# Performance work log

Hardware: AMD Instinct MI355X
Metric: run time of the kernel (lower is better)

The kernel has to match this reference:

```python
import jax, jax.numpy as jnp
import numpy as np

K = 10          # neighbors per span
KTOK = 3        # heads used per span
D = 2.0         # token adjacency threshold
GAMMA = 1.0
MAX_WIDTH = 16
CAP = 128       # cap_spans_per_token
B, L, KTOK_TOTAL = 8, 128, 4


def _enumerate_spans(L, max_width):
    ar = np.arange(L)
    l_g, r_g = np.meshgrid(ar, ar, indexing='ij')
    mask = (r_g >= l_g) & (r_g - l_g + 1 <= max_width)
    l_idx = l_g[mask]
    r_idx = r_g[mask]
    S = l_idx.size
    span2id = np.full((L, L), -1, dtype=np.int64)
    span2id[l_idx, r_idx] = np.arange(S)
    return span2id, l_idx, r_idx, S


def _geom_matrix(L, max_width, span2id, l_idx, r_idx):
    # 8-neighborhood (l+/-1, r+/-1) adjacency over span ids, boolean (S,S)
    S = l_idx.size
    off = np.array([[-1, -1], [-1, 0], [-1, 1], [0, -1], [0, 1], [1, -1], [1, 0], [1, 1]])
    nl = l_idx[:, None] + off[None, :, 0]
    nr = r_idx[:, None] + off[None, :, 1]
    valid = (nl >= 0) & (nr >= 0) & (nl <= nr) & (nr < L) & (nr - nl + 1 <= max_width)
    s2 = span2id[np.clip(nl, 0, L - 1), np.clip(nr, 0, L - 1)]
    rows = np.broadcast_to(np.arange(S)[:, None], s2.shape)
    m = valid & (s2 >= 0)
    Geom = np.zeros((S, S), dtype=bool)
    Geom[rows[m], s2[m]] = True
    np.fill_diagonal(Geom, False)
    return Geom


SPAN2ID, L_IDX, R_IDX, S = _enumerate_spans(L, MAX_WIDTH)
GEOM = jnp.asarray(_geom_matrix(L, MAX_WIDTH, SPAN2ID, L_IDX, R_IDX))


def setup_inputs() -> dict:
    key = jax.random.key(0)
    k1, k2, k3 = jax.random.split(key, 3)
    head_indices = jax.random.randint(k1, (B, L, L, KTOK_TOTAL), 0, L)
    head_weights = jax.random.uniform(k2, (B, L, L, KTOK_TOTAL), dtype=jnp.float32)
    dist = jax.random.uniform(k3, (B, L, L), dtype=jnp.float32) * 8.0
    return {"head_indices": head_indices, "head_weights": head_weights, "dist": dist}


def reference(head_indices, head_weights, dist):
    l_idx = jnp.asarray(L_IDX)
    r_idx = jnp.asarray(R_IDX)
    # gather per-span head indices/weights: (B, S, Ktok)
    idx_all = head_indices[:, l_idx, r_idx, :KTOK]
    w_all = head_weights[:, l_idx, r_idx, :KTOK]
    valid1 = idx_all >= 0
    idx_safe = jnp.clip(idx_all, 0, None)
    w_all = w_all * valid1.astype(w_all.dtype)

    # scatter-add token->span dense matrices: (B, S, L)
    b_ix = jnp.arange(B)[:, None, None]
    s_ix = jnp.arange(S)[None, :, None]
    P_w = jnp.zeros((B, S, L), w_all.dtype).at[b_ix, s_ix, idx_safe].add(w_all)
    P_bin = jnp.zeros((B, S, L), jnp.float32).at[b_ix, s_ix, idx_safe].add(valid1.astype(jnp.float32))

    # token adjacency with self loops
    A = jnp.maximum((dist <= D).astype(jnp.float32), jnp.eye(L, dtype=jnp.float32))
    U_mask = jnp.einsum('bsl,blm->bsm', P_bin, A) > 0.0  # (B, S, L) spans hitting token m

    # top-1 head token -> span one-hot, with per-token span cap
    top1 = jnp.clip(idx_all[:, :, 0], 0, L - 1)
    top1_valid = (idx_all[:, :, 0] >= 0).astype(jnp.float32)
    E = jax.nn.one_hot(top1, L, dtype=jnp.float32) * top1_valid[..., None]  # (B, S, L)
    E = jnp.swapaxes(E, 1, 2)  # (B, L, S)
    E = E * (jnp.cumsum(E, axis=2) <= float(CAP)).astype(jnp.float32)

    # candidate matrix M: (B, S, S)
    M = jnp.einsum('bsl,blt->bst', U_mask.astype(jnp.float32), E) > 0.0
    diag = jnp.arange(S)
    M = M.at[:, diag, diag].set(False)
    M = M | GEOM[None]

    # gate scores Gate = P_w @ exp(-gamma*dist) @ P_w^T
    G = jnp.exp(-GAMMA * dist)
    A_pw = jnp.einsum('bsl,blm->bsm', P_w, G)
    Gate = jnp.einsum('bsm,btm->bst', A_pw, P_w)

    Gate_masked = jnp.where(M, Gate, -jnp.inf)
    topk_vals, topk_idx = jax.lax.top_k(Gate_masked, K)  # (B, S, K)
    N_mask = jnp.isfinite(topk_vals)
    N_idx = topk_idx.astype(jnp.int32)

    # self-loop fill for invalid slots
    rows = jnp.broadcast_to(jnp.arange(S, dtype=N_idx.dtype)[None, :, None], (B, S, K))
    N_idx = jnp.where(N_mask, N_idx, rows)
    N_mask = jnp.ones_like(N_mask)
    return N_idx, N_mask
```

## Files before the change

### kernel.cpp

```cpp
#include <hip/hip_runtime.h>
#include <stdint.h>

#define NB 8
#define LL 128
#define NS 1928
#define NK 10
#define WPB 4

__device__ __forceinline__ int span_id(int l, int r) {
    int off = (l <= 112) ? (l << 4) : (NS - (((128 - l) * (129 - l)) >> 1));
    return off + (r - l);
}

__device__ __forceinline__ float npexp_f32(float x) {
    const float magic = 12582912.0f;
    const float log2e = 1.442695040888963f;
    const float c1 = -6.93145752e-1f;
    const float c2 = -1.42860677e-6f;
    float t = __fmul_rn(x, log2e);
    float q = __fsub_rn(__fadd_rn(t, magic), magic);
    float r = __fmaf_rn(q, c1, x);
    r = __fmaf_rn(q, c2, r);
    float num = __fmaf_rn(r, 5.082762527590693718096e-04f, 6.757896990527504603057e-03f);
    num = __fmaf_rn(num, r, 5.114512081637298353406e-02f);
    num = __fmaf_rn(num, r, 2.473615434895520810817e-01f);
    num = __fmaf_rn(num, r, 7.257664613233124478488e-01f);
    num = __fmaf_rn(num, r, 9.999999999980870924916e-01f);
    float den = __fmaf_rn(r, 2.159509375685829852307e-02f, -2.742335390411667452936e-01f);
    den = __fmaf_rn(den, r, 1.0f);
    float p = __fdiv_rn(num, den);
    int qi = (int)q;
    return __fmul_rn(p, __int_as_float((127 + qi) << 23));
}

__device__ __forceinline__ float keyval(unsigned long long k) {
    return __uint_as_float((unsigned)(k >> 32));
}

__device__ __forceinline__ void wfence() {
    __builtin_amdgcn_wave_barrier();
    __threadfence_block();
    __builtin_amdgcn_wave_barrier();
}

__device__ int wave_partition_fast(unsigned long long* a, int* posL, int* posR,
                                   int pl, int pr, int lane) {
    int pm = pl + ((pr - pl) >> 1);
    unsigned long long vl = a[pl], vm = a[pm], vr = a[pr], tt;
    if (keyval(vm) < keyval(vl)) { tt = vm; vm = vl; vl = tt; }
    if (keyval(vr) < keyval(vm)) { tt = vr; vr = vm; vm = tt; }
    if (keyval(vm) < keyval(vl)) { tt = vm; vm = vl; vl = tt; }
    float vp = keyval(vm);
    unsigned long long vq = a[pr - 1];
    if (lane == 0) { a[pl] = vl; a[pr] = vr; a[pm] = vq; a[pr - 1] = vm; }
    wfence();

    unsigned long long lmask = (1ull << lane) - 1ull;
    int baseL = 0, baseR = 0;
    for (int p0 = pl; p0 <= pr; p0 += 64) {
        int pos = p0 + lane;
        bool inr = (pos <= pr);
        float v = inr ? keyval(a[pos]) : 0.0f;
        bool ge = inr && (pos > pl) && (pos < pr) && (v >= vp);
        bool le = inr && (pos <= pr - 2) && (v <= vp);
        unsigned long long bge = __ballot(ge);
        unsigned long long ble = __ballot(le);
        if (ge) posL[baseL + __popcll(bge & lmask)] = pos;
        if (le) posR[baseR + __popcll(ble & lmask)] = pos;
        baseL += __popcll(bge);
        baseR += __popcll(ble);
    }
    wfence();
    int totGE = baseL, totLE = baseR;
    int maxk = (totGE < totLE) ? totGE : totLE;
    int K = 0;
    for (int base = 0;; base += 64) {
        int k = base + lane;
        bool active = (k < maxk);
        int Lk = active ? posL[k] : 0x7fffffff;
        int Rk = active ? posR[totLE - 1 - k] : -1;
        bool sw = active && (Lk < Rk);
        unsigned long long bm = __ballot(sw);
        int nsw = (~bm == 0ull) ? 64 : (__ffsll((long long)~bm) - 1);
        if (sw && (lane < nsw)) {
            unsigned long long tl = a[Lk], tr = a[Rk];
            a[Lk] = tr; a[Rk] = tl;
        }
        K += nsw;
        if (nsw < 64) break;
    }
    wfence();
    int pi = posL[K];
    if (K > 0) { int rp = posR[totLE - K]; if (rp < pi) pi = rp; }
    if (lane == 0) { tt = a[pi]; a[pi] = a[pr - 1]; a[pr - 1] = tt; }
    wfence();
    return pi;
}

__device__ __forceinline__ void lane_sift(unsigned long long* h, int start, int hm) {
    unsigned long long tmp = h[start];
    int i = start, j = start + start;
    while (j <= hm) {
        if (j < hm && keyval(h[j]) < keyval(h[j + 1])) ++j;
        if (keyval(tmp) < keyval(h[j])) { h[i] = h[j]; i = j; j += j; }
        else break;
    }
    h[i] = tmp;
}

__device__ void wave_heap_top(unsigned long long* a, int lo, int hi, int needlo, int lane) {
    unsigned long long* h = a + lo - 1;
    int hm = hi - lo + 1;
    int half = hm >> 1;
    int maxlvl = 0; { int v = half; while (v >>= 1) ++maxlvl; }
    for (int lvl = maxlvl; lvl >= 0; --lvl) {
        int n0 = 1 << lvl;
        int n1 = (n0 << 1) - 1; if (n1 > half) n1 = half;
        for (int nb = n0; nb <= n1; nb += 64) {
            int node = nb + lane;
            if (node <= n1) lane_sift(h, node, hm);
        }
        wfence();
    }
    int E = hi - needlo + 1;
    if (E > hm - 1) E = hm - 1;
    if (lane == 0) {
        int m = hm;
        for (int e = 0; e < E; ++e) {
            unsigned long long tmp = h[m]; h[m] = h[1]; --m;
            int i = 1, j = 2;
            while (j <= m) {
                if (j < m && keyval(h[j]) < keyval(h[j + 1])) ++j;
                if (keyval(tmp) < keyval(h[j])) { h[i] = h[j]; i = j; j += j; }
                else break;
            }
            h[i] = tmp;
        }
    }
    wfence();
}

__device__ void wave_insertion(unsigned long long* a, int lo, int hi, int lane) {
    int len = hi - lo + 1;
    unsigned long long v = (lane < len) ? a[lo + lane] : 0ull;
    float fv = keyval(v);
    int rank = 0;
    for (int j = 0; j < len; ++j) {
        unsigned long long vj = __shfl(v, j, 64);
        float fj = keyval(vj);
        if ((fj < fv) || (fj == fv && j < lane)) ++rank;
    }
    wfence();
    if (lane < len) a[lo + rank] = v;
    wfence();
}

__device__ void wave_np_sort_top(unsigned long long* a, int n, int lane, int* stk,
                                 int* posL, int* posR) {
    int depth = 0; { int v = n; while (v >>= 1) ++depth; }
    depth *= 2;
    const int TOPLO = n - NK;
    int sp = 0;
    int lo = 0, hi = n - 1;
    for (;;) {
        while (hi - lo > 15) {
            if (depth-- < 0) {
                if (hi >= TOPLO) wave_heap_top(a, lo, hi, (lo > TOPLO ? lo : TOPLO), lane);
                goto pop;
            }
            {
                int pi = wave_partition_fast(a, posL, posR, lo, hi, lane);
                if (pi - lo < hi - pi) {
                    if (lane == 0) { stk[sp * 2] = pi + 1; stk[sp * 2 + 1] = hi; }
                    ++sp; hi = pi - 1;
                } else {
                    if (lane == 0) { stk[sp * 2] = lo; stk[sp * 2 + 1] = pi - 1; }
                    ++sp; lo = pi + 1;
                }
                wfence();
            }
        }
        if (hi > lo && hi >= TOPLO) wave_insertion(a, lo, hi, lane);
pop:
        if (sp == 0) break;
        --sp;
        lo = stk[sp * 2]; hi = stk[sp * 2 + 1];
    }
}

__global__ void top1_kernel(const int* __restrict__ hi,
                            unsigned char* __restrict__ top1,
                            unsigned char* __restrict__ flags) {
    int tid = blockIdx.x * blockDim.x + threadIdx.x;
    if (tid >= NB * NS) return;
    int b = tid / NS, t = tid - b * NS;
    int l, r;
    if (t < 1808) { l = t >> 4; r = l + (t & 15); }
    else {
        l = 113;
        while (l < 127 && span_id(l + 1, l + 1) <= t) ++l;
        r = l + (t - span_id(l, l));
    }
    int i0 = hi[((b * LL + l) * LL + r) * 4];
    top1[b * NS + t] = (unsigned char)(i0 & 127);
    flags[b * NS + t] = 0;
}

__global__ void cap_kernel(const unsigned char* __restrict__ top1,
                           unsigned char* __restrict__ flags) {
    int gw = (blockIdx.x * blockDim.x + threadIdx.x) >> 6;
    int lane = threadIdx.x & 63;
    int b = gw >> 7, l = gw & 127;
    const unsigned char* tb = top1 + b * NS;
    unsigned char* fb = flags + b * NS;
    int cnt = 0;
    for (int t0 = 0; t0 < NS; t0 += 64) {
        int t = t0 + lane;
        int tp = (t < NS) ? (int)tb[t] : 255;
        bool match = (tp == l);
        unsigned long long m = __ballot(match);
        if (match) {
            int pre = __popcll(m & ((1ull << lane) - 1ull));
            fb[t] = (cnt + pre + 1 <= 128) ? 1 : 0;
        }
        cnt += __popcll(m);
    }
}

__device__ __forceinline__ void stage_tables(const int* hb, const float* wb,
                                             const unsigned char* fb,
                                             float4* s_pack, uint16_t* s_lrc) {
    for (int j = threadIdx.x; j < LL * 16; j += 256) {
        int l = j >> 4, w = j & 15, r = l + w;
        if (r < LL) {
            int sid = span_id(l, r);
            int4 iv = *(const int4*)(hb + (l * LL + r) * 4);
            float4 wv = *(const float4*)(wb + (l * LL + r) * 4);
            int ia = iv.x, ib = iv.y, ic = iv.z;
            float wa = wv.x, wb2 = wv.y, wc = wv.z;
            int m0, m1 = 255, m2 = 255;
            float W0, W1 = 0.f, W2 = 0.f;
            if (ia == ib && ib == ic) {
                m0 = ia; W0 = __fadd_rn(__fadd_rn(wa, wb2), wc);
            } else if (ia == ib) {
                float W = __fadd_rn(wa, wb2);
                if (ia < ic) { m0 = ia; W0 = W; m1 = ic; W1 = wc; }
                else         { m0 = ic; W0 = wc; m1 = ia; W1 = W; }
            } else if (ia == ic) {
                float W = __fadd_rn(wa, wc);
                if (ia < ib) { m0 = ia; W0 = W; m1 = ib; W1 = wb2; }
                else         { m0 = ib; W0 = wb2; m1 = ia; W1 = W; }
            } else if (ib == ic) {
                float W = __fadd_rn(wb2, wc);
                if (ia < ib) { m0 = ia; W0 = wa; m1 = ib; W1 = W; }
                else         { m0 = ib; W0 = W; m1 = ia; W1 = wa; }
            } else {
                int x0 = ia, x1 = ib, x2 = ic; float y0 = wa, y1 = wb2, y2 = wc;
                if (x0 > x1) { int tx = x0; x0 = x1; x1 = tx; float ty = y0; y0 = y1; y1 = ty; }
                if (x1 > x2) { int tx = x1; x1 = x2; x2 = tx; float ty = y1; y1 = y2; y2 = ty; }
                if (x0 > x1) { int tx = x0; x0 = x1; x1 = tx; float ty = y0; y0 = y1; y1 = ty; }
                m0 = x0; m1 = x1; m2 = x2; W0 = y0; W1 = y1; W2 = y2;
            }
            uint32_t cap = fb[sid] & 1u;
            uint32_t rec = (uint32_t)m0 | ((uint32_t)m1 << 8) | ((uint32_t)m2 << 16)
                         | ((uint32_t)(ia & 127) << 24);
            s_pack[sid] = make_float4(W0, W1, W2, __uint_as_float(rec));
            s_lrc[sid] = (uint16_t)(l | (r << 7) | (cap << 14));
        }
    }
}

__global__ __launch_bounds__(256)
void span_scan_kernel(const int* __restrict__ hi, const float* __restrict__ hw,
                      const float* __restrict__ dist,
                      const unsigned char* __restrict__ capf,
                      unsigned char* __restrict__ rowflag,
                      int* __restrict__ out) {
    __shared__ float4 s_pack[NS];
    __shared__ uint16_t s_lrc[NS];
    __shared__ float s_q[WPB][LL];

    const int b = blockIdx.y;
    stage_tables(hi + b * LL * LL * 4, hw + b * LL * LL * 4, capf + b * NS, s_pack, s_lrc);
    __syncthreads();

    const int wid = threadIdx.x >> 6;
    const int lane = threadIdx.x & 63;
    const int s = blockIdx.x * WPB + wid;

    float4 ps = s_pack[s];
    uint32_t rec = __float_as_uint(ps.w);
    int m0 = rec & 255, m1 = (rec >> 8) & 255, m2 = (rec >> 16) & 255;
    bool e1 = (m1 != 255), e2 = (m2 != 255);
    uint32_t lrc = s_lrc[s];
    int ls = lrc & 127, rs = (lrc >> 7) & 127;

    const float* db = dist + b * LL * LL;
    const float* row0 = db + m0 * LL;
    const float* row1 = db + (e1 ? m1 : 0) * LL;
    const float* row2 = db + (e2 ? m2 : 0) * LL;
    int mA = lane, mB = lane + 64;
    float dA0 = row0[mA], dB0 = row0[mB];
    float dA1 = row1[mA], dB1 = row1[mB];
    float dA2 = row2[mA], dB2 = row2[mB];
    float qA = __fmaf_rn(ps.x, npexp_f32(-dA0), 0.0f);
    qA = __fmaf_rn(ps.y, npexp_f32(-dA1), qA);
    qA = __fmaf_rn(ps.z, npexp_f32(-dA2), qA);
    float qB = __fmaf_rn(ps.x, npexp_f32(-dB0), 0.0f);
    qB = __fmaf_rn(ps.y, npexp_f32(-dB1), qB);
    qB = __fmaf_rn(ps.z, npexp_f32(-dB2), qB);
    bool cA = (dA0 <= 2.0f || mA == m0) ||
              (e1 && (dA1 <= 2.0f || mA == m1)) ||
              (e2 && (dA2 <= 2.0f || mA == m2));
    bool cB = (dB0 <= 2.0f || mB == m0) ||
              (e1 && (dB1 <= 2.0f || mB == m1)) ||
              (e2 && (dB2 <= 2.0f || mB == m2));
    unsigned long long ub0 = __ballot(cA);
    unsigned long long ub1 = __ballot(cB);
    s_q[wid][mA] = qA;
    s_q[wid][mB] = qB;
    const float* q = s_q[wid];

    unsigned v = 0u; int vi = -1; unsigned tau = 0u;

    for (int t0 = 0; t0 < NS; t0 += 64) {
        int t = t0 + lane;
        unsigned key = 0u;
        if (t < NS) {
            float4 pt = s_pack[t];
            uint32_t rt = __float_as_uint(pt.w);
            float g = __fmaf_rn(pt.x, q[rt & 127], 0.0f);
            g = __fmaf_rn(pt.y, q[(rt >> 8) & 127], g);
            g = __fmaf_rn(pt.z, q[(rt >> 16) & 127], g);
            uint32_t lr = s_lrc[t];
            int lt = lr & 127, rt2 = (lr >> 7) & 127;
            int dl = lt - ls; if (dl < 0) dl = -dl;
            int dr = rt2 - rs; if (dr < 0) dr = -dr;
            bool neq = (t != s);
            bool geom = neq && (dl <= 1) && (dr <= 1);
            int ri0 = rt >> 24;
            unsigned long long bits = (ri0 & 64) ? ub1 : ub0;
            bool um = (((bits >> (ri0 & 63)) & 1ull) != 0) && ((lr >> 14) & 1u) && neq;
            if (um || geom) key = __float_as_uint(g);
        }
        unsigned long long bm = __ballot(key > tau);
        while (bm) {
            int ln = __ffsll((long long)bm) - 1;
            bm &= bm - 1;
            unsigned kk = __shfl(key, ln, 64);
            if (kk > tau) {
                int tk = t0 + ln;
                unsigned vprev = __shfl_up(v, 1, 64);
                int iprev = __shfl_up(vi, 1, 64);
                if (lane == 0) vprev = 0xFFFFFFFFu;
                bool keep = (v >= kk);
                bool fp = (vprev < kk);
                v = keep ? v : (fp ? vprev : kk);
                vi = keep ? vi : (fp ? iprev : tk);
                tau = __shfl(v, 10, 64);
            }
        }
    }

    unsigned vn = __shfl_down(v, 1, 64);
    bool tie = (lane < NK) && (v != 0u) && (vn == v);
    bool flag = (__ballot(tie) != 0ull);

    if (lane < NK) {
        int o = (b * NS + s) * NK + lane;
        out[NB * NS * NK + o] = 1;
        if (!flag) out[o] = (vi >= 0) ? vi : s;
    }
    if (lane == 0) rowflag[b * NS + s] = flag ? 1 : 0;
}

__global__ __launch_bounds__(256)
void span_slow_kernel(const int* __restrict__ hi, const float* __restrict__ hw,
                      const float* __restrict__ dist,
                      const unsigned char* __restrict__ capf,
                      const unsigned char* __restrict__ rowflag,
                      int* __restrict__ out) {
    __shared__ int s_nrows;
    __shared__ int s_rows[256];
    __shared__ float4 s_pack[NS];
    __shared__ uint16_t s_lrc[NS];
    __shared__ float s_qq[LL];
    __shared__ unsigned long long s_cov[2];
    __shared__ unsigned long long s_buf[NS];
    __shared__ int s_posL[NS], s_posR[NS];
    __shared__ int s_stk[48];

    const int b = blockIdx.x;
    if (threadIdx.x == 0) s_nrows = 0;
    __syncthreads();
    for (int i = threadIdx.x; i < NS; i += 256) {
        if (rowflag[b * NS + i]) {
            int k = atomicAdd(&s_nrows, 1);
            if (k < 256) s_rows[k] = i;
        }
    }
    __syncthreads();
    int nrows = s_nrows; if (nrows > 256) nrows = 256;
    if (nrows == 0) return;

    stage_tables(hi + b * LL * LL * 4, hw + b * LL * LL * 4, capf + b * NS, s_pack, s_lrc);
    __syncthreads();

    const int wid = threadIdx.x >> 6;
    const int lane = threadIdx.x & 63;
    const float* db = dist + b * LL * LL;

    for (int ri = 0; ri < nrows; ++ri) {
        const int s = s_rows[ri];
        uint32_t lrc = s_lrc[s];
        int ls = lrc & 127, rs = (lrc >> 7) & 127;

        if (wid == 0) {
            float4 ps = s_pack[s];
            uint32_t rec = __float_as_uint(ps.w);
            int m0 = rec & 255, m1 = (rec >> 8) & 255, m2 = (rec >> 16) & 255;
            bool e1 = (m1 != 255), e2 = (m2 != 255);
            const float* row0 = db + m0 * LL;
            const float* row1 = db + (e1 ? m1 : 0) * LL;
            const float* row2 = db + (e2 ? m2 : 0) * LL;
            int mA = lane, mB = lane + 64;
            float dA0 = row0[mA], dB0 = row0[mB];
            float dA1 = row1[mA], dB1 = row1[mB];
            float dA2 = row2[mA], dB2 = row2[mB];
            float qA = __fmaf_rn(ps.x, npexp_f32(-dA0), 0.0f);
            qA = __fmaf_rn(ps.y, npexp_f32(-dA1), qA);
            qA = __fmaf_rn(ps.z, npexp_f32(-dA2), qA);
            float qB = __fmaf_rn(ps.x, npexp_f32(-dB0), 0.0f);
            qB = __fmaf_rn(ps.y, npexp_f32(-dB1), qB);
            qB = __fmaf_rn(ps.z, npexp_f32(-dB2), qB);
            bool cA = (dA0 <= 2.0f || mA == m0) ||
                      (e1 && (dA1 <= 2.0f || mA == m1)) ||
                      (e2 && (dA2 <= 2.0f || mA == m2));
            bool cB = (dB0 <= 2.0f || mB == m0) ||
                      (e1 && (dB1 <= 2.0f || mB == m1)) ||
                      (e2 && (dB2 <= 2.0f || mB == m2));
            unsigned long long u0 = __ballot(cA);
            unsigned long long u1 = __ballot(cB);
            s_qq[mA] = qA;
            s_qq[mB] = qB;
            if (lane == 0) { s_cov[0] = u0; s_cov[1] = u1; }
        }
        __syncthreads();
        unsigned long long ub0 = s_cov[0], ub1 = s_cov[1];

        for (int t = threadIdx.x; t < NS; t += 256) {
            float4 pt = s_pack[t];
            uint32_t rt = __float_as_uint(pt.w);
            float g = __fmaf_rn(pt.x, s_qq[rt & 127], 0.0f);
            g = __fmaf_rn(pt.y, s_qq[(rt >> 8) & 127], g);
            g = __fmaf_rn(pt.z, s_qq[(rt >> 16) & 127], g);
            uint32_t lr = s_lrc[t];
            int lt = lr & 127, rt2 = (lr >> 7) & 127;
            int dl = lt - ls; if (dl < 0) dl = -dl;
            int dr = rt2 - rs; if (dr < 0) dr = -dr;
            bool neq = (t != s);
            bool geom = neq && (dl <= 1) && (dr <= 1);
            int ri0 = rt >> 24;
            unsigned long long bits = (ri0 & 64) ? ub1 : ub0;
            bool um = (((bits >> (ri0 & 63)) & 1ull) != 0) && ((lr >> 14) & 1u) && neq;
            unsigned h32 = (um || geom) ? __float_as_uint(g) : 0xFF800000u;
            s_buf[t] = ((unsigned long long)h32 << 32) | (unsigned)t;
        }
        __syncthreads();

        if (wid == 0) {
            wave_np_sort_top(s_buf, NS, lane, s_stk, s_posL, s_posR);
            if (lane < NK) {
                unsigned long long k = s_buf[NS - 1 - lane];
                int idx = ((unsigned)(k >> 32) == 0xFF800000u) ? s : (int)(k & 0xffffffffull);
                out[(b * NS + s) * NK + lane] = idx;
            }
        }
        __syncthreads();
    }
}

extern "C" void kernel_launch(void* const* d_in, const int* in_sizes, int n_in,
                              void* d_out, int out_size, void* d_ws, size_t ws_size,
                              hipStream_t stream) {
    const int* hi = (const int*)d_in[0];
    const float* hw = (const float*)d_in[1];
    const float* dist = (const float*)d_in[2];
    int* out = (int*)d_out;

    unsigned char* ws = (unsigned char*)d_ws;
    unsigned char* top1 = ws;
    unsigned char* capf = ws + NB * NS;
    unsigned char* rowflag = ws + 2 * NB * NS;

    int n1 = NB * NS;
    top1_kernel<<<(n1 + 255) / 256, 256, 0, stream>>>(hi, top1, capf);
    cap_kernel<<<(NB * LL * 64) / 256, 256, 0, stream>>>(top1, capf);
    dim3 grid(NS / WPB, NB);
    span_scan_kernel<<<grid, 256, 0, stream>>>(hi, hw, dist, capf, rowflag, out);
    span_slow_kernel<<<NB, 256, 0, stream>>>(hi, hw, dist, capf, rowflag, out);
}
```

Measured before the change: 239.5 us.

## Precompute span tables once globally and process two spans per wave

Adds a build_tables kernel that computes the per-span packed head and weight records once and writes them to workspace. The scan and slow kernels now copy these tables into shared memory instead of rebuilding them from the raw inputs in every block. Each wave now handles two spans, so every shared-memory read of a candidate record serves two gate and mask evaluations, and the grid is halved. The cost is more registers, two serial top-k merges per wave, and fewer blocks, which may reduce occupancy.

```diff
diff --git a/kernel.cpp b/kernel.cpp
--- a/kernel.cpp
+++ b/kernel.cpp
@@ -6,6 +6,7 @@
 #define NS 1928
 #define NK 10
 #define WPB 4
+#define SPW 2
 
 __device__ __forceinline__ int span_id(int l, int r) {
     int off = (l <= 112) ? (l << 4) : (NS - (((128 - l) * (129 - l)) >> 1));
@@ -188,22 +189,51 @@
     }
 }
 
-__global__ void top1_kernel(const int* __restrict__ hi,
-                            unsigned char* __restrict__ top1,
-                            unsigned char* __restrict__ flags) {
-    int tid = blockIdx.x * blockDim.x + threadIdx.x;
-    if (tid >= NB * NS) return;
-    int b = tid / NS, t = tid - b * NS;
-    int l, r;
-    if (t < 1808) { l = t >> 4; r = l + (t & 15); }
-    else {
-        l = 113;
-        while (l < 127 && span_id(l + 1, l + 1) <= t) ++l;
-        r = l + (t - span_id(l, l));
-    }
-    int i0 = hi[((b * LL + l) * LL + r) * 4];
-    top1[b * NS + t] = (unsigned char)(i0 & 127);
-    flags[b * NS + t] = 0;
+__global__ __launch_bounds__(256)
+void build_tables_kernel(const int* __restrict__ hi, const float* __restrict__ hw,
+                         float4* __restrict__ g_pack, uint16_t* __restrict__ g_lrc,
+                         unsigned char* __restrict__ top1) {
+    int j = blockIdx.x * 256 + threadIdx.x;
+    if (j >= NB * LL * 16) return;
+    int b = j >> 11;
+    int lw = j & 2047;
+    int l = lw >> 4, w = lw & 15, r = l + w;
+    if (r >= LL) return;
+    int sid = span_id(l, r);
+    const int* hb = hi + b * LL * LL * 4;
+    const float* wb = hw + b * LL * LL * 4;
+    int4 iv = *(const int4*)(hb + (l * LL + r) * 4);
+    float4 wv = *(const float4*)(wb + (l * LL + r) * 4);
+    int ia = iv.x, ib = iv.y, ic = iv.z;
+    float wa = wv.x, wb2 = wv.y, wc = wv.z;
+    int m0, m1 = 255, m2 = 255;
+    float W0, W1 = 0.f, W2 = 0.f;
+    if (ia == ib && ib == ic) {
+        m0 = ia; W0 = __fadd_rn(__fadd_rn(wa, wb2), wc);
+    } else if (ia == ib) {
+        float W = __fadd_rn(wa, wb2);
+        if (ia < ic) { m0 = ia; W0 = W; m1 = ic; W1 = wc; }
+        else         { m0 = ic; W0 = wc; m1 = ia; W1 = W; }
+    } else if (ia == ic) {
+        float W = __fadd_rn(wa, wc);
+        if (ia < ib) { m0 = ia; W0 = W; m1 = ib; W1 = wb2; }
+        else         { m0 = ib; W0 = wb2; m1 = ia; W1 = W; }
+    } else if (ib == ic) {
+        float W = __fadd_rn(wb2, wc);
+        if (ia < ib) { m0 = ia; W0 = wa; m1 = ib; W1 = W; }
+        else         { m0 = ib; W0 = W; m1 = ia; W1 = wa; }
+    } else {
+        int x0 = ia, x1 = ib, x2 = ic; float y0 = wa, y1 = wb2, y2 = wc;
+        if (x0 > x1) { int tx = x0; x0 = x1; x1 = tx; float ty = y0; y0 = y1; y1 = ty; }
+        if (x1 > x2) { int tx = x1; x1 = x2; x2 = tx; float ty = y1; y1 = y2; y2 = ty; }
+        if (x0 > x1) { int tx = x0; x0 = x1; x1 = tx; float ty = y0; y0 = y1; y1 = ty; }
+        m0 = x0; m1 = x1; m2 = x2; W0 = y0; W1 = y1; W2 = y2;
+    }
+    uint32_t rec = (uint32_t)m0 | ((uint32_t)m1 << 8) | ((uint32_t)m2 << 16)
+                 | ((uint32_t)(ia & 127) << 24);
+    g_pack[b * NS + sid] = make_float4(W0, W1, W2, __uint_as_float(rec));
+    g_lrc[b * NS + sid] = (uint16_t)(l | (r << 7));
+    top1[b * NS + sid] = (unsigned char)(ia & 127);
 }
 
 __global__ void cap_kernel(const unsigned char* __restrict__ top1,
@@ -227,75 +257,22 @@
     }
 }
 
-__device__ __forceinline__ void stage_tables(const int* hb, const float* wb,
-                                             const unsigned char* fb,
-                                             float4* s_pack, uint16_t* s_lrc) {
-    for (int j = threadIdx.x; j < LL * 16; j += 256) {
-        int l = j >> 4, w = j & 15, r = l + w;
-        if (r < LL) {
-            int sid = span_id(l, r);
-            int4 iv = *(const int4*)(hb + (l * LL + r) * 4);
-            float4 wv = *(const float4*)(wb + (l * LL + r) * 4);
-            int ia = iv.x, ib = iv.y, ic = iv.z;
-            float wa = wv.x, wb2 = wv.y, wc = wv.z;
-            int m0, m1 = 255, m2 = 255;
-            float W0, W1 = 0.f, W2 = 0.f;
-            if (ia == ib && ib == ic) {
-                m0 = ia; W0 = __fadd_rn(__fadd_rn(wa, wb2), wc);
-            } else if (ia == ib) {
-                float W = __fadd_rn(wa, wb2);
-                if (ia < ic) { m0 = ia; W0 = W; m1 = ic; W1 = wc; }
-                else         { m0 = ic; W0 = wc; m1 = ia; W1 = W; }
-            } else if (ia == ic) {
-                float W = __fadd_rn(wa, wc);
-                if (ia < ib) { m0 = ia; W0 = W; m1 = ib; W1 = wb2; }
-                else         { m0 = ib; W0 = wb2; m1 = ia; W1 = W; }
-            } else if (ib == ic) {
-                float W = __fadd_rn(wb2, wc);
-                if (ia < ib) { m0 = ia; W0 = wa; m1 = ib; W1 = W; }
-                else         { m0 = ib; W0 = W; m1 = ia; W1 = wa; }
-            } else {
-                int x0 = ia, x1 = ib, x2 = ic; float y0 = wa, y1 = wb2, y2 = wc;
-                if (x0 > x1) { int tx = x0; x0 = x1; x1 = tx; float ty = y0; y0 = y1; y1 = ty; }
-                if (x1 > x2) { int tx = x1; x1 = x2; x2 = tx; float ty = y1; y1 = y2; y2 = ty; }
-                if (x0 > x1) { int tx = x0; x0 = x1; x1 = tx; float ty = y0; y0 = y1; y1 = ty; }
-                m0 = x0; m1 = x1; m2 = x2; W0 = y0; W1 = y1; W2 = y2;
-            }
-            uint32_t cap = fb[sid] & 1u;
-            uint32_t rec = (uint32_t)m0 | ((uint32_t)m1 << 8) | ((uint32_t)m2 << 16)
-                         | ((uint32_t)(ia & 127) << 24);
-            s_pack[sid] = make_float4(W0, W1, W2, __uint_as_float(rec));
-            s_lrc[sid] = (uint16_t)(l | (r << 7) | (cap << 14));
-        }
-    }
-}
-
-__global__ __launch_bounds__(256)
-void span_scan_kernel(const int* __restrict__ hi, const float* __restrict__ hw,
-                      const float* __restrict__ dist,
-                      const unsigned char* __restrict__ capf,
-                      unsigned char* __restrict__ rowflag,
-                      int* __restrict__ out) {
-    __shared__ float4 s_pack[NS];
-    __shared__ uint16_t s_lrc[NS];
-    __shared__ float s_q[WPB][LL];
-
-    const int b = blockIdx.y;
-    stage_tables(hi + b * LL * LL * 4, hw + b * LL * LL * 4, capf + b * NS, s_pack, s_lrc);
-    __syncthreads();
-
-    const int wid = threadIdx.x >> 6;
-    const int lane = threadIdx.x & 63;
-    const int s = blockIdx.x * WPB + wid;
-
-    float4 ps = s_pack[s];
+__device__ __forceinline__ void load_tables(const float4* __restrict__ gp,
+                                            const uint16_t* __restrict__ gl,
+                                            const unsigned char* __restrict__ fb,
+                                            float4* s_pack, uint16_t* s_lrc) {
+    for (int j = threadIdx.x; j < NS; j += 256) {
+        s_pack[j] = gp[j];
+        s_lrc[j] = (uint16_t)(gl[j] | ((fb[j] & 1) << 14));
+    }
+}
+
+__device__ __forceinline__ void span_prologue(const float* __restrict__ db, float4 ps,
+                                              int lane, float* qrow,
+                                              unsigned long long* ub) {
     uint32_t rec = __float_as_uint(ps.w);
     int m0 = rec & 255, m1 = (rec >> 8) & 255, m2 = (rec >> 16) & 255;
     bool e1 = (m1 != 255), e2 = (m2 != 255);
-    uint32_t lrc = s_lrc[s];
-    int ls = lrc & 127, rs = (lrc >> 7) & 127;
-
-    const float* db = dist + b * LL * LL;
     const float* row0 = db + m0 * LL;
     const float* row1 = db + (e1 ? m1 : 0) * LL;
     const float* row2 = db + (e2 ? m2 : 0) * LL;
@@ -315,57 +292,39 @@
     bool cB = (dB0 <= 2.0f || mB == m0) ||
               (e1 && (dB1 <= 2.0f || mB == m1)) ||
               (e2 && (dB2 <= 2.0f || mB == m2));
-    unsigned long long ub0 = __ballot(cA);
-    unsigned long long ub1 = __ballot(cB);
-    s_q[wid][mA] = qA;
-    s_q[wid][mB] = qB;
-    const float* q = s_q[wid];
-
-    unsigned v = 0u; int vi = -1; unsigned tau = 0u;
-
-    for (int t0 = 0; t0 < NS; t0 += 64) {
-        int t = t0 + lane;
-        unsigned key = 0u;
-        if (t < NS) {
-            float4 pt = s_pack[t];
-            uint32_t rt = __float_as_uint(pt.w);
-            float g = __fmaf_rn(pt.x, q[rt & 127], 0.0f);
-            g = __fmaf_rn(pt.y, q[(rt >> 8) & 127], g);
-            g = __fmaf_rn(pt.z, q[(rt >> 16) & 127], g);
-            uint32_t lr = s_lrc[t];
-            int lt = lr & 127, rt2 = (lr >> 7) & 127;
-            int dl = lt - ls; if (dl < 0) dl = -dl;
-            int dr = rt2 - rs; if (dr < 0) dr = -dr;
-            bool neq = (t != s);
-            bool geom = neq && (dl <= 1) && (dr <= 1);
-            int ri0 = rt >> 24;
-            unsigned long long bits = (ri0 & 64) ? ub1 : ub0;
-            bool um = (((bits >> (ri0 & 63)) & 1ull) != 0) && ((lr >> 14) & 1u) && neq;
-            if (um || geom) key = __float_as_uint(g);
-        }
-        unsigned long long bm = __ballot(key > tau);
-        while (bm) {
-            int ln = __ffsll((long long)bm) - 1;
-            bm &= bm - 1;
-            unsigned kk = __shfl(key, ln, 64);
-            if (kk > tau) {
-                int tk = t0 + ln;
-                unsigned vprev = __shfl_up(v, 1, 64);
-                int iprev = __shfl_up(vi, 1, 64);
-                if (lane == 0) vprev = 0xFFFFFFFFu;
-                bool keep = (v >= kk);
-                bool fp = (vprev < kk);
-                v = keep ? v : (fp ? vprev : kk);
-                vi = keep ? vi : (fp ? iprev : tk);
-                tau = __shfl(v, 10, 64);
-            }
-        }
-    }
-
+    ub[0] = __ballot(cA);
+    ub[1] = __ballot(cB);
+    qrow[mA] = qA;
+    qrow[mB] = qB;
+}
+
+__device__ __forceinline__ void topk_merge(unsigned key, int t0, int lane,
+                                           unsigned& v, int& vi, unsigned& tau) {
+    unsigned long long bm = __ballot(key > tau);
+    while (bm) {
+        int ln = __ffsll((long long)bm) - 1;
+        bm &= bm - 1;
+        unsigned kk = __shfl(key, ln, 64);
+        if (kk > tau) {
+            int tk = t0 + ln;
+            unsigned vprev = __shfl_up(v, 1, 64);
+            int iprev = __shfl_up(vi, 1, 64);
+            if (lane == 0) vprev = 0xFFFFFFFFu;
+            bool keep = (v >= kk);
+            bool fp = (vprev < kk);
+            v = keep ? v : (fp ? vprev : kk);
+            vi = keep ? vi : (fp ? iprev : tk);
+            tau = __shfl(v, 10, 64);
+        }
+    }
+}
+
+__device__ __forceinline__ void span_epilogue(unsigned v, int vi, int b, int s, int lane,
+                                              unsigned char* __restrict__ rowflag,
+                                              int* __restrict__ out) {
     unsigned vn = __shfl_down(v, 1, 64);
     bool tie = (lane < NK) && (v != 0u) && (vn == v);
     bool flag = (__ballot(tie) != 0ull);
-
     if (lane < NK) {
         int o = (b * NS + s) * NK + lane;
         out[NB * NS * NK + o] = 1;
@@ -375,7 +334,90 @@
 }
 
 __global__ __launch_bounds__(256)
-void span_slow_kernel(const int* __restrict__ hi, const float* __restrict__ hw,
+void span_scan_kernel(const float4* __restrict__ g_pack,
+                      const uint16_t* __restrict__ g_lrc,
+                      const float* __restrict__ dist,
+                      const unsigned char* __restrict__ capf,
+                      unsigned char* __restrict__ rowflag,
+                      int* __restrict__ out) {
+    __shared__ float4 s_pack[NS];
+    __shared__ uint16_t s_lrc[NS];
+    __shared__ float s_q[WPB][SPW][LL];
+
+    const int b = blockIdx.y;
+    load_tables(g_pack + b * NS, g_lrc + b * NS, capf + b * NS, s_pack, s_lrc);
+    __syncthreads();
+
+    const int wid = threadIdx.x >> 6;
+    const int lane = threadIdx.x & 63;
+    const int base = blockIdx.x * (WPB * SPW);
+    const int sA = base + wid;
+    const int sB = base + WPB + wid;
+
+    const float* db = dist + b * LL * LL;
+    unsigned long long ubA0, ubA1, ubB0, ubB1;
+    {
+        unsigned long long ub[2];
+        span_prologue(db, s_pack[sA], lane, s_q[wid][0], ub);
+        ubA0 = ub[0]; ubA1 = ub[1];
+        span_prologue(db, s_pack[sB], lane, s_q[wid][1], ub);
+        ubB0 = ub[0]; ubB1 = ub[1];
+    }
+    uint32_t lrcA = s_lrc[sA], lrcB = s_lrc[sB];
+    int lsA = lrcA & 127, rsA = (lrcA >> 7) & 127;
+    int lsB = lrcB & 127, rsB = (lrcB >> 7) & 127;
+    const float* qa = s_q[wid][0];
+    const float* qb = s_q[wid][1];
+
+    unsigned vA = 0u, vB = 0u; int viA = -1, viB = -1; unsigned tauA = 0u, tauB = 0u;
+
+    for (int t0 = 0; t0 < NS; t0 += 64) {
+        int t = t0 + lane;
+        unsigned keyA = 0u, keyB = 0u;
+        if (t < NS) {
+            float4 pt = s_pack[t];
+            uint32_t rt = __float_as_uint(pt.w);
+            int i0 = rt & 127, i1 = (rt >> 8) & 127, i2 = (rt >> 16) & 127;
+            uint32_t lr = s_lrc[t];
+            int lt = lr & 127, rt2 = (lr >> 7) & 127;
+            int ri0 = rt >> 24;
+            bool capb = ((lr >> 14) & 1u) != 0;
+            {
+                float g = __fmaf_rn(pt.x, qa[i0], 0.0f);
+                g = __fmaf_rn(pt.y, qa[i1], g);
+                g = __fmaf_rn(pt.z, qa[i2], g);
+                int dl = lt - lsA; if (dl < 0) dl = -dl;
+                int dr = rt2 - rsA; if (dr < 0) dr = -dr;
+                bool neq = (t != sA);
+                bool geom = neq && (dl <= 1) && (dr <= 1);
+                unsigned long long bits = (ri0 & 64) ? ubA1 : ubA0;
+                bool um = (((bits >> (ri0 & 63)) & 1ull) != 0) && capb && neq;
+                if (um || geom) keyA = __float_as_uint(g);
+            }
+            {
+                float g = __fmaf_rn(pt.x, qb[i0], 0.0f);
+                g = __fmaf_rn(pt.y, qb[i1], g);
+                g = __fmaf_rn(pt.z, qb[i2], g);
+                int dl = lt - lsB; if (dl < 0) dl = -dl;
+                int dr = rt2 - rsB; if (dr < 0) dr = -dr;
+                bool neq = (t != sB);
+                bool geom = neq && (dl <= 1) && (dr <= 1);
+                unsigned long long bits = (ri0 & 64) ? ubB1 : ubB0;
+                bool um = (((bits >> (ri0 & 63)) & 1ull) != 0) && capb && neq;
+                if (um || geom) keyB = __float_as_uint(g);
+            }
+        }
+        topk_merge(keyA, t0, lane, vA, viA, tauA);
+        topk_merge(keyB, t0, lane, vB, viB, tauB);
+    }
+
+    span_epilogue(vA, viA, b, sA, lane, rowflag, out);
+    span_epilogue(vB, viB, b, sB, lane, rowflag, out);
+}
+
+__global__ __launch_bounds__(256)
+void span_slow_kernel(const float4* __restrict__ g_pack,
+                      const uint16_t* __restrict__ g_lrc,
                       const float* __restrict__ dist,
                       const unsigned char* __restrict__ capf,
                       const unsigned char* __restrict__ rowflag,
@@ -403,7 +445,7 @@
     int nrows = s_nrows; if (nrows > 256) nrows = 256;
     if (nrows == 0) return;
 
-    stage_tables(hi + b * LL * LL * 4, hw + b * LL * LL * 4, capf + b * NS, s_pack, s_lrc);
+    load_tables(g_pack + b * NS, g_lrc + b * NS, capf + b * NS, s_pack, s_lrc);
     __syncthreads();
 
     const int wid = threadIdx.x >> 6;
@@ -416,34 +458,9 @@
         int ls = lrc & 127, rs = (lrc >> 7) & 127;
 
         if (wid == 0) {
-            float4 ps = s_pack[s];
-            uint32_t rec = __float_as_uint(ps.w);
-            int m0 = rec & 255, m1 = (rec >> 8) & 255, m2 = (rec >> 16) & 255;
-            bool e1 = (m1 != 255), e2 = (m2 != 255);
-            const float* row0 = db + m0 * LL;
-            const float* row1 = db + (e1 ? m1 : 0) * LL;
-            const float* row2 = db + (e2 ? m2 : 0) * LL;
-            int mA = lane, mB = lane + 64;
-            float dA0 = row0[mA], dB0 = row0[mB];
-            float dA1 = row1[mA], dB1 = row1[mB];
-            float dA2 = row2[mA], dB2 = row2[mB];
-            float qA = __fmaf_rn(ps.x, npexp_f32(-dA0), 0.0f);
-            qA = __fmaf_rn(ps.y, npexp_f32(-dA1), qA);
-            qA = __fmaf_rn(ps.z, npexp_f32(-dA2), qA);
-            float qB = __fmaf_rn(ps.x, npexp_f32(-dB0), 0.0f);
-            qB = __fmaf_rn(ps.y, npexp_f32(-dB1), qB);
-            qB = __fmaf_rn(ps.z, npexp_f32(-dB2), qB);
-            bool cA = (dA0 <= 2.0f || mA == m0) ||
-                      (e1 && (dA1 <= 2.0f || mA == m1)) ||
-                      (e2 && (dA2 <= 2.0f || mA == m2));
-            bool cB = (dB0 <= 2.0f || mB == m0) ||
-                      (e1 && (dB1 <= 2.0f || mB == m1)) ||
-                      (e2 && (dB2 <= 2.0f || mB == m2));
-            unsigned long long u0 = __ballot(cA);
-            unsigned long long u1 = __ballot(cB);
-            s_qq[mA] = qA;
-            s_qq[mB] = qB;
-            if (lane == 0) { s_cov[0] = u0; s_cov[1] = u1; }
+            unsigned long long ub[2];
+            span_prologue(db, s_pack[s], lane, s_qq, ub);
+            if (lane == 0) { s_cov[0] = ub[0]; s_cov[1] = ub[1]; }
         }
         __syncthreads();
         unsigned long long ub0 = s_cov[0], ub1 = s_cov[1];
@@ -492,11 +509,12 @@
     unsigned char* top1 = ws;
     unsigned char* capf = ws + NB * NS;
     unsigned char* rowflag = ws + 2 * NB * NS;
-
-    int n1 = NB * NS;
-    top1_kernel<<<(n1 + 255) / 256, 256, 0, stream>>>(hi, top1, capf);
+    float4* g_pack = (float4*)(ws + 3 * NB * NS);
+    uint16_t* g_lrc = (uint16_t*)(ws + 3 * NB * NS + NB * NS * 16);
+
+    build_tables_kernel<<<(NB * LL * 16) / 256, 256, 0, stream>>>(hi, hw, g_pack, g_lrc, top1);
     cap_kernel<<<(NB * LL * 64) / 256, 256, 0, stream>>>(top1, capf);
-    dim3 grid(NS / WPB, NB);
-    span_scan_kernel<<<grid, 256, 0, stream>>>(hi, hw, dist, capf, rowflag, out);
-    span_slow_kernel<<<NB, 256, 0, stream>>>(hi, hw, dist, capf, rowflag, out);
-}
+    dim3 grid(NS / (WPB * SPW), NB);
+    span_scan_kernel<<<grid, 256, 0, stream>>>(g_pack, g_lrc, dist, capf, rowflag, out);
+    span_slow_kernel<<<NB, 256, 0, stream>>>(g_pack, g_lrc, dist, capf, rowflag, out);
+}
```

Measured after the change: 214.1 us. 10.6% less time.
